# Performance work log

Measured on AMD Instinct MI355X. Metric: run time of the kernel, lower is better.

The kernel has to match this reference:

```python
import jax, jax.numpy as jnp
import numpy as np

B, S, H, L = 32, 2048, 256, 2


def setup_inputs() -> dict:
    key = jax.random.key(0)
    k = jax.random.split(key, 5)
    scale = 1.0 / np.sqrt(H)  # torch-style uniform-ish init scale, use scaled normal
    return {
        "inputs": jax.random.normal(k[0], (B, S, H), dtype=jnp.float32),
        "h0": jnp.zeros((L, B, H), dtype=jnp.float32),
        "W_ih": jax.random.normal(k[1], (L, H, H), dtype=jnp.float32) * scale,
        "W_hh": jax.random.normal(k[2], (L, H, H), dtype=jnp.float32) * scale,
        "b_ih": jax.random.normal(k[3], (L, H), dtype=jnp.float32) * scale,
        "b_hh": jax.random.normal(k[4], (L, H), dtype=jnp.float32) * scale,
    }


def reference(inputs, h0, W_ih, W_hh, b_ih, b_hh):
    """Multi-layer unidirectional Elman RNN (tanh), batch_first, delay=1.

    Matches BaseRNN/RNNLayer: per timestep out, h_new = cell(x_t, h);
    with a vanilla cell out == h_new = tanh(x W_ih^T + b_ih + h W_hh^T + b_hh).
    Returns (outputs [B,S,H] of last layer, final hidden [L,B,H]).
    """
    x = inputs
    finals = []
    n_layers = W_ih.shape[0]
    for l in range(n_layers):  # small fixed loop over layers
        # hoist the input projection out of the recurrence: [B,S,H]
        xp = jnp.einsum("bsi,hi->bsh", x, W_ih[l]) + b_ih[l]
        Whh_l = W_hh[l]
        bhh_l = b_hh[l]

        def step(h, xt):
            h_new = jnp.tanh(xt + h @ Whh_l.T + bhh_l)
            return h_new, h_new

        h_last, ys = jax.lax.scan(step, h0[l], jnp.swapaxes(xp, 0, 1))  # ys: [S,B,H]
        x = jnp.swapaxes(ys, 0, 1)  # [B,S,H]
        finals.append(h_last)
    return x, jnp.stack(finals, axis=0)
```

## Files before the change

kernel.cpp:

```cpp
#include <hip/hip_runtime.h>
#include <cstddef>

#define Bn 32
#define Sn 2048
#define Hn 256
#define Ln 2
#define CHUNK 64
#define NCHUNK (Sn / CHUNK)

#define PSTR 10
#define PBUF (Hn * PSTR)

#define FPAD 32
#define NFL (5 * Bn)

typedef float f32x2 __attribute__((ext_vector_type(2)));

__device__ unsigned g_flags[NFL * FPAD];

__global__ void zero_flags_k() {
  int i = threadIdx.x;
  if (i < NFL)
    __hip_atomic_store(&g_flags[i * FPAD], 0u, __ATOMIC_RELAXED,
                       __HIP_MEMORY_SCOPE_AGENT);
}

__device__ __forceinline__ float tanh_fast(float x) {
  float e = __expf(2.0f * x);
  return 1.0f - 2.0f / (e + 1.0f);
}

__device__ __forceinline__ float ldg_dev(const float* p) {
  return __hip_atomic_load(p, __ATOMIC_RELAXED, __HIP_MEMORY_SCOPE_AGENT);
}
__device__ __forceinline__ void stg_dev(float* p, float v) {
  __hip_atomic_store(p, v, __ATOMIC_RELAXED, __HIP_MEMORY_SCOPE_AGENT);
}

__device__ __forceinline__ void poll_ge_n(unsigned* base, int n, unsigned tgt) {
  for (int q = 0; q < n; ++q) {
    unsigned* f = base + (size_t)q * Bn * FPAD;
    while (__hip_atomic_load(f, __ATOMIC_RELAXED, __HIP_MEMORY_SCOPE_AGENT) < tgt)
      __builtin_amdgcn_s_sleep(2);
  }
}

__device__ __forceinline__ void publish(unsigned* f, unsigned val, int t) {
  asm volatile("s_waitcnt vmcnt(0)" ::: "memory");
  __syncthreads();
  if (t == 0)
    __hip_atomic_store(f, val, __ATOMIC_RELAXED, __HIP_MEMORY_SCOPE_AGENT);
}

template <bool XP_SC1, bool Y_SC1>
__device__ void rec_body(const float* __restrict__ xp_b,
                         const float* __restrict__ Whh,
                         const float* __restrict__ bhh,
                         const float* __restrict__ h0_b,
                         float* __restrict__ y_b,
                         float* __restrict__ hfin_b,
                         unsigned* wbase, int nw, unsigned* pub,
                         float* part, float* hbuf) {
  const int t = threadIdx.x;
  const int lane = t & 63;
  const int w = t >> 6;
  const int ocol = 32 * w + (lane & 31);

  f32x2 Wreg[4][16];
#pragma unroll
  for (int r = 0; r < 4; ++r)
#pragma unroll
    for (int q = 0; q < 8; ++q) {
      float4 v = *(const float4*)&Whh[(size_t)(lane + 64 * r) * Hn + 32 * w + 4 * q];
      Wreg[r][2 * q + 0] = f32x2{v.x, v.y};
      Wreg[r][2 * q + 1] = f32x2{v.z, v.w};
    }
#pragma unroll
  for (int r = 0; r < 4; ++r)
#pragma unroll
    for (int c = 0; c < 16; ++c)
      asm("" : "+v"(Wreg[r][c]));

  const int pw0 = PSTR * lane + (w ^ ((lane >> 3) & 3));
  const float bias = bhh[ocol];

  f32x2 hv[16];
#pragma unroll
  for (int j = 0; j < 8; ++j) {
    float4 v = *(const float4*)&h0_b[32 * w + 4 * j];
    hv[2 * j + 0] = f32x2{v.x, v.y};
    hv[2 * j + 1] = f32x2{v.z, v.w};
  }

  for (int c = 0; c < NCHUNK; ++c) {
    if (t == 0) poll_ge_n(wbase, nw, c + 1);
    __syncthreads();

    const int s0 = c * CHUNK;
    float xp_cur = ldg_dev(&xp_b[(size_t)s0 * Hn + ocol]);
    float xp_n1  = ldg_dev(&xp_b[(size_t)(s0 + 1) * Hn + ocol]);

    for (int ss = 0; ss < CHUNK; ++ss) {
      const int s = s0 + ss;
      float xp_n2 = 0.0f;
      if (s + 2 < Sn)
        xp_n2 = XP_SC1 ? ldg_dev(&xp_b[(size_t)(s + 2) * Hn + ocol])
                       : xp_b[(size_t)(s + 2) * Hn + ocol];

      f32x2 acc0 = {0.f, 0.f}, acc1 = {0.f, 0.f};
      f32x2 acc2 = {0.f, 0.f}, acc3 = {0.f, 0.f};
#pragma unroll
      for (int cc = 0; cc < 16; ++cc) {
        asm("v_pk_fma_f32 %0, %1, %2, %0" : "+v"(acc0) : "v"(Wreg[0][cc]), "v"(hv[cc]));
        asm("v_pk_fma_f32 %0, %1, %2, %0" : "+v"(acc1) : "v"(Wreg[1][cc]), "v"(hv[cc]));
        asm("v_pk_fma_f32 %0, %1, %2, %0" : "+v"(acc2) : "v"(Wreg[2][cc]), "v"(hv[cc]));
        asm("v_pk_fma_f32 %0, %1, %2, %0" : "+v"(acc3) : "v"(Wreg[3][cc]), "v"(hv[cc]));
      }
      float* pbuf = &part[(s & 1) * PBUF];
      pbuf[pw0       ] = acc0.x + acc0.y;
      pbuf[pw0 +  640] = acc1.x + acc1.y;
      pbuf[pw0 + 1280] = acc2.x + acc2.y;
      pbuf[pw0 + 1920] = acc3.x + acc3.y;

      asm volatile("s_waitcnt lgkmcnt(0)" ::: "memory");
      __builtin_amdgcn_s_barrier();
      __builtin_amdgcn_sched_barrier(0);

      const f32x2* prow = (const f32x2*)&pbuf[PSTR * ocol];
      f32x2 p0 = prow[0], p1 = prow[1], p2 = prow[2], p3 = prow[3];
      f32x2 q01 = p0 + p1;
      f32x2 q23 = p2 + p3;
      f32x2 qq = q01 + q23;
      float hn = tanh_fast((qq.x + qq.y) + xp_cur + bias);
      if (lane < 32) {
        hbuf[ocol] = hn;
        if (Y_SC1) stg_dev(&y_b[(size_t)s * Hn + ocol], hn);
        else       y_b[(size_t)s * Hn + ocol] = hn;
      }
      xp_cur = xp_n1;
      xp_n1 = xp_n2;

      __builtin_amdgcn_wave_barrier();
#pragma unroll
      for (int j = 0; j < 8; ++j) {
        float4 v = *(const float4*)&hbuf[32 * w + 4 * j];
        hv[2 * j + 0] = f32x2{v.x, v.y};
        hv[2 * j + 1] = f32x2{v.z, v.w};
      }
    }

    if (pub) publish(pub, (unsigned)(c + 1), t);
  }

  if (lane < 32) hfin_b[ocol] = hbuf[ocol];
}

__device__ void proj_body(const float* __restrict__ Ab,
                          const float* __restrict__ W,
                          const float* __restrict__ bias,
                          float* __restrict__ Cb,
                          unsigned* waitf, unsigned* pub,
                          int nt0, int nt1,
                          float* smem) {
  const int t = threadIdx.x;
  const int tx = t & 15;
  const int ty = t >> 4;
  float (*As)[68] = (float(*)[68])smem;
  float (*Bs)[68] = (float(*)[68])(smem + 64 * 68);

  for (int c = 0; c < NCHUNK; ++c) {
    if (waitf) {
      if (t == 0) poll_ge_n(waitf, 1, c + 1);
      __syncthreads();
    }
    const float* A = Ab + (size_t)(c * CHUNK) * Hn;
    float* C = Cb + (size_t)(c * CHUNK) * Hn;

    for (int nt = nt0; nt < nt1; ++nt) {
      const int n0 = nt * 64;
      float acc[2][4] = {{0.f, 0.f, 0.f, 0.f}, {0.f, 0.f, 0.f, 0.f}};
      for (int kc = 0; kc < Hn; kc += 64) {
#pragma unroll
        for (int r = 0; r < 2; ++r) {
          int idx = t + 512 * r;
          int mm = idx >> 4;
          int kk = (idx & 15) << 2;
          float4 av = *(const float4*)&A[(size_t)mm * Hn + kc + kk];
          As[kk + 0][mm] = av.x; As[kk + 1][mm] = av.y;
          As[kk + 2][mm] = av.z; As[kk + 3][mm] = av.w;
          float4 wv = *(const float4*)&W[(size_t)(n0 + mm) * Hn + kc + kk];
          Bs[kk + 0][mm] = wv.x; Bs[kk + 1][mm] = wv.y;
          Bs[kk + 2][mm] = wv.z; Bs[kk + 3][mm] = wv.w;
        }
        __syncthreads();
#pragma unroll
        for (int k = 0; k < 64; ++k) {
          float a0 = As[k][2 * ty], a1 = As[k][2 * ty + 1];
          float4 bv = *(const float4*)&Bs[k][tx << 2];
          acc[0][0] += a0 * bv.x; acc[0][1] += a0 * bv.y;
          acc[0][2] += a0 * bv.z; acc[0][3] += a0 * bv.w;
          acc[1][0] += a1 * bv.x; acc[1][1] += a1 * bv.y;
          acc[1][2] += a1 * bv.z; acc[1][3] += a1 * bv.w;
        }
        __syncthreads();
      }
      float4 bb = *(const float4*)&bias[n0 + (tx << 2)];
#pragma unroll
      for (int i = 0; i < 2; ++i) {
        float* cp = &C[(size_t)(2 * ty + i) * Hn + n0 + (tx << 2)];
        stg_dev(cp + 0, acc[i][0] + bb.x);
        stg_dev(cp + 1, acc[i][1] + bb.y);
        stg_dev(cp + 2, acc[i][2] + bb.z);
        stg_dev(cp + 3, acc[i][3] + bb.w);
      }
    }

    publish(pub, (unsigned)(c + 1), t);
  }
}

__global__ __launch_bounds__(512)
__attribute__((amdgpu_waves_per_eu(2, 2)))
void fused(
    const float* __restrict__ x, const float* __restrict__ h0,
    const float* __restrict__ Wih, const float* __restrict__ Whh,
    const float* __restrict__ bih, const float* __restrict__ bhh,
    float* __restrict__ yout, float* __restrict__ fin,
    float* __restrict__ xpws) {
  __shared__ float smem[2 * 64 * 68];
  const int bid = blockIdx.x;

  if (bid < 32) {
    const int b = bid;
    rec_body<false, true>(xpws + (size_t)b * Sn * Hn, Whh, bhh,
                          h0 + (size_t)b * Hn,
                          yout + (size_t)b * Sn * Hn, fin + (size_t)b * Hn,
                          &g_flags[(0 * Bn + b) * FPAD], 2,
                          &g_flags[(2 * Bn + b) * FPAD],
                          smem, smem + 2 * PBUF);
  } else if (bid < 64) {
    const int b = bid - 32;
    rec_body<true, false>(xpws + (size_t)b * Sn * Hn, Whh + Hn * Hn, bhh + Hn,
                          h0 + (size_t)Bn * Hn + (size_t)b * Hn,
                          yout + (size_t)b * Sn * Hn,
                          fin + (size_t)Bn * Hn + (size_t)b * Hn,
                          &g_flags[(3 * Bn + b) * FPAD], 2, nullptr,
                          smem, smem + 2 * PBUF);
  } else if (bid < 128) {
    const int q = bid - 64;
    const int b = q & 31, j = q >> 5;
    proj_body(x + (size_t)b * Sn * Hn, Wih, bih, xpws + (size_t)b * Sn * Hn,
              nullptr, &g_flags[((0 + j) * Bn + b) * FPAD],
              2 * j, 2 * j + 2, smem);
  } else {
    const int q = bid - 128;
    const int b = q & 31, j = q >> 5;
    proj_body(yout + (size_t)b * Sn * Hn, Wih + Hn * Hn, bih + Hn,
              xpws + (size_t)b * Sn * Hn,
              &g_flags[(2 * Bn + b) * FPAD],
              &g_flags[((3 + j) * Bn + b) * FPAD],
              2 * j, 2 * j + 2, smem);
  }
}

extern "C" void kernel_launch(void* const* d_in, const int* in_sizes, int n_in,
                              void* d_out, int out_size, void* d_ws, size_t ws_size,
                              hipStream_t stream) {
  const float* x   = (const float*)d_in[0];
  const float* h0  = (const float*)d_in[1];
  const float* Wih = (const float*)d_in[2];
  const float* Whh = (const float*)d_in[3];
  const float* bih = (const float*)d_in[4];
  const float* bhh = (const float*)d_in[5];

  float* out = (float*)d_out;
  float* yout = out;
  float* fin  = out + (size_t)Bn * Sn * Hn;
  float* xpws = (float*)d_ws;

  zero_flags_k<<<1, 256, 0, stream>>>();
  fused<<<192, 512, 0, stream>>>(x, h0, Wih, Whh, bih, bhh, yout, fin, xpws);
}
```

Measured before the change: 1.757 ms.

## Halve chunk size, pace layer-0 projection behind recurrence, lengthen poll sleep

Halves the time chunk from 64 to 32 steps so the recurrence blocks can start sooner and hand work to downstream blocks at a finer grain. The projection tile is reshaped to one row per thread-row to match. Layer-0 projection blocks are now throttled to stay at most PACE chunks ahead of the layer-0 recurrence, which reduces contention for memory and compute. Spin-wait sleep is lengthened to cut polling traffic, but this may add wake-up latency to every handoff. The finer chunks also double the number of flag handoffs and shrink each GEMM tile, which lowers arithmetic intensity.

```diff
diff --git a/kernel.cpp b/kernel.cpp
--- a/kernel.cpp
+++ b/kernel.cpp
@@ -5,8 +5,9 @@
 #define Sn 2048
 #define Hn 256
 #define Ln 2
-#define CHUNK 64
+#define CHUNK 32
 #define NCHUNK (Sn / CHUNK)
+#define PACE 2
 
 #define PSTR 10
 #define PBUF (Hn * PSTR)
@@ -41,7 +42,7 @@
   for (int q = 0; q < n; ++q) {
     unsigned* f = base + (size_t)q * Bn * FPAD;
     while (__hip_atomic_load(f, __ATOMIC_RELAXED, __HIP_MEMORY_SCOPE_AGENT) < tgt)
-      __builtin_amdgcn_s_sleep(2);
+      __builtin_amdgcn_s_sleep(32);
   }
 }
 
@@ -159,18 +160,21 @@
                           const float* __restrict__ W,
                           const float* __restrict__ bias,
                           float* __restrict__ Cb,
-                          unsigned* waitf, unsigned* pub,
+                          unsigned* waitf, unsigned* pace, unsigned* pub,
                           int nt0, int nt1,
                           float* smem) {
   const int t = threadIdx.x;
   const int tx = t & 15;
   const int ty = t >> 4;
-  float (*As)[68] = (float(*)[68])smem;
-  float (*Bs)[68] = (float(*)[68])(smem + 64 * 68);
+  float (*As)[34] = (float(*)[34])smem;
+  float (*Bs)[68] = (float(*)[68])(smem + 64 * 34);
 
   for (int c = 0; c < NCHUNK; ++c) {
-    if (waitf) {
-      if (t == 0) poll_ge_n(waitf, 1, c + 1);
+    if (waitf || pace) {
+      if (t == 0) {
+        if (waitf) poll_ge_n(waitf, 1, c + 1);
+        if (pace && c > PACE) poll_ge_n(pace, 1, (unsigned)(c - PACE));
+      }
       __syncthreads();
     }
     const float* A = Ab + (size_t)(c * CHUNK) * Hn;
@@ -178,16 +182,20 @@
 
     for (int nt = nt0; nt < nt1; ++nt) {
       const int n0 = nt * 64;
-      float acc[2][4] = {{0.f, 0.f, 0.f, 0.f}, {0.f, 0.f, 0.f, 0.f}};
+      float acc[4] = {0.f, 0.f, 0.f, 0.f};
       for (int kc = 0; kc < Hn; kc += 64) {
+        {
+          int mm = t >> 4;
+          int kk = (t & 15) << 2;
+          float4 av = *(const float4*)&A[(size_t)mm * Hn + kc + kk];
+          As[kk + 0][mm] = av.x; As[kk + 1][mm] = av.y;
+          As[kk + 2][mm] = av.z; As[kk + 3][mm] = av.w;
+        }
 #pragma unroll
         for (int r = 0; r < 2; ++r) {
           int idx = t + 512 * r;
           int mm = idx >> 4;
           int kk = (idx & 15) << 2;
-          float4 av = *(const float4*)&A[(size_t)mm * Hn + kc + kk];
-          As[kk + 0][mm] = av.x; As[kk + 1][mm] = av.y;
-          As[kk + 2][mm] = av.z; As[kk + 3][mm] = av.w;
           float4 wv = *(const float4*)&W[(size_t)(n0 + mm) * Hn + kc + kk];
           Bs[kk + 0][mm] = wv.x; Bs[kk + 1][mm] = wv.y;
           Bs[kk + 2][mm] = wv.z; Bs[kk + 3][mm] = wv.w;
@@ -195,24 +203,19 @@
         __syncthreads();
 #pragma unroll
         for (int k = 0; k < 64; ++k) {
-          float a0 = As[k][2 * ty], a1 = As[k][2 * ty + 1];
+          float a = As[k][ty];
           float4 bv = *(const float4*)&Bs[k][tx << 2];
-          acc[0][0] += a0 * bv.x; acc[0][1] += a0 * bv.y;
-          acc[0][2] += a0 * bv.z; acc[0][3] += a0 * bv.w;
-          acc[1][0] += a1 * bv.x; acc[1][1] += a1 * bv.y;
-          acc[1][2] += a1 * bv.z; acc[1][3] += a1 * bv.w;
+          acc[0] += a * bv.x; acc[1] += a * bv.y;
+          acc[2] += a * bv.z; acc[3] += a * bv.w;
         }
         __syncthreads();
       }
       float4 bb = *(const float4*)&bias[n0 + (tx << 2)];
-#pragma unroll
-      for (int i = 0; i < 2; ++i) {
-        float* cp = &C[(size_t)(2 * ty + i) * Hn + n0 + (tx << 2)];
-        stg_dev(cp + 0, acc[i][0] + bb.x);
-        stg_dev(cp + 1, acc[i][1] + bb.y);
-        stg_dev(cp + 2, acc[i][2] + bb.z);
-        stg_dev(cp + 3, acc[i][3] + bb.w);
-      }
+      float* cp = &C[(size_t)ty * Hn + n0 + (tx << 2)];
+      stg_dev(cp + 0, acc[0] + bb.x);
+      stg_dev(cp + 1, acc[1] + bb.y);
+      stg_dev(cp + 2, acc[2] + bb.z);
+      stg_dev(cp + 3, acc[3] + bb.w);
     }
 
     publish(pub, (unsigned)(c + 1), t);
@@ -250,14 +253,15 @@
     const int q = bid - 64;
     const int b = q & 31, j = q >> 5;
     proj_body(x + (size_t)b * Sn * Hn, Wih, bih, xpws + (size_t)b * Sn * Hn,
-              nullptr, &g_flags[((0 + j) * Bn + b) * FPAD],
+              nullptr, &g_flags[(2 * Bn + b) * FPAD],
+              &g_flags[((0 + j) * Bn + b) * FPAD],
               2 * j, 2 * j + 2, smem);
   } else {
     const int q = bid - 128;
     const int b = q & 31, j = q >> 5;
     proj_body(yout + (size_t)b * Sn * Hn, Wih + Hn * Hn, bih + Hn,
               xpws + (size_t)b * Sn * Hn,
-              &g_flags[(2 * Bn + b) * FPAD],
+              &g_flags[(2 * Bn + b) * FPAD], nullptr,
               &g_flags[((3 + j) * Bn + b) * FPAD],
               2 * j, 2 * j + 2, smem);
   }
```

New measurement: 1.759 ms. About the same (+0.1%).
